# Kernel tuning notes

Hardware: AMD Instinct MI355X
Metric: run time of the kernel (lower is better)

Reference implementation:

```python
import jax, jax.numpy as jnp
import numpy as np

NEG_SLOPE = 0.2
HEADS = 8

def _gat_conv(x, src, dst, n_nodes, W, att_src, att_dst, bias):
    # x: [N, Fin], W: [Fin, H*C], att_*: [H, C], bias: [C]
    H, C = att_src.shape
    xl = (x @ W).reshape(n_nodes, H, C)                      # [N,H,C]
    a_src = (xl * att_src[None]).sum(-1)                      # [N,H]
    a_dst = (xl * att_dst[None]).sum(-1)                      # [N,H]
    e = jax.nn.leaky_relu(a_src[src] + a_dst[dst], NEG_SLOPE) # [E,H]
    m = jax.ops.segment_max(e, dst, num_segments=n_nodes)     # [N,H]
    ee = jnp.exp(e - m[dst])
    s = jax.ops.segment_sum(ee, dst, num_segments=n_nodes)    # [N,H]
    alpha = ee / s[dst]                                       # [E,H]
    msg = alpha[:, :, None] * xl[src]                         # [E,H,C]
    out = jax.ops.segment_sum(msg, dst, num_segments=n_nodes) # [N,H,C]
    return out.mean(axis=1) + bias                            # [N,C] (concat=False)

def setup_inputs() -> dict:
    key = jax.random.key(0)
    ks = jax.random.split(key, 12)
    N, E, EL = 50000, 800000, 200000
    V, D, HID, OUT = 5000, 128, 32, 32
    inp = {}
    inp['x'] = jax.random.randint(ks[0], (N,), 0, V)
    inp['edge_index'] = jax.random.randint(ks[1], (2, E), 0, N)
    inp['edge_label_index'] = jax.random.randint(ks[2], (2, EL), 0, N)
    inp['emb'] = jax.random.normal(ks[3], (V, D), jnp.float32) * D ** -0.5
    inp['W1'] = jax.random.normal(ks[4], (D, HEADS * HID), jnp.float32) * D ** -0.5
    inp['att_src1'] = jax.random.normal(ks[5], (HEADS, HID), jnp.float32) * HID ** -0.5
    inp['att_dst1'] = jax.random.normal(ks[6], (HEADS, HID), jnp.float32) * HID ** -0.5
    inp['b1'] = jnp.zeros((HID,), jnp.float32)
    inp['W2'] = jax.random.normal(ks[7], (HID, HEADS * OUT), jnp.float32) * HID ** -0.5
    inp['att_src2'] = jax.random.normal(ks[8], (HEADS, OUT), jnp.float32) * OUT ** -0.5
    inp['att_dst2'] = jax.random.normal(ks[9], (HEADS, OUT), jnp.float32) * OUT ** -0.5
    inp['b2'] = jnp.zeros((OUT,), jnp.float32)
    return inp

def reference(x, edge_index, edge_label_index, emb, W1, att_src1, att_dst1, b1, W2, att_src2, att_dst2, b2):
    N = x.shape[0]
    # PyG GATConv adds self-loops by default
    loop = jnp.arange(N)
    src = jnp.concatenate([edge_index[0], loop])
    dst = jnp.concatenate([edge_index[1], loop])
    h = emb[x]                                                   # [N, D] embedding lookup (squeeze(1) equivalent)
    h = jax.nn.relu(_gat_conv(h, src, dst, N, W1, att_src1, att_dst1, b1))
    # dropout p=0.5 is identity at inference (training=False)
    z = _gat_conv(h, src, dst, N, W2, att_src2, att_dst2, b2)    # [N, OUT]
    # decode: dot product over label edges
    return (z[edge_label_index[0]] * z[edge_label_index[1]]).sum(axis=-1)
```

## Files before the change

### kernel.cpp

```cpp
#include <hip/hip_runtime.h>
#include <hip/hip_fp16.h>
#include <math.h>
#include <limits.h>

#define HH 8
#define CC 32
#define NEG 0.2f

struct __align__(8) half4 { __half2 a, b; };
typedef float f32x4 __attribute__((ext_vector_type(4)));

__device__ __forceinline__ int ldnt(const int* p){ return __builtin_nontemporal_load(p); }
__device__ __forceinline__ float ldntf(const float* p){ return __builtin_nontemporal_load(p); }
__device__ __forceinline__ f32x4 ldnt4(const float* p){ return __builtin_nontemporal_load((const f32x4*)p); }
__device__ __forceinline__ void stnt4(float* p, f32x4 v){ __builtin_nontemporal_store(v, (f32x4*)p); }
__device__ __forceinline__ int f2ord(float f){ int i=__float_as_int(f); return i>=0? i : i^0x7fffffff; }
__device__ __forceinline__ float ord2f(int i){ return __int_as_float(i>=0? i : i^0x7fffffff); }

__device__ __forceinline__ void edge_sd_nt(const int* __restrict__ ei, int e, int E, int& s, int& d){
  if(e < E){ s = ldnt(ei+e); d = ldnt(ei+E+e); } else { s = e-E; d = s; }
}

__global__ void k_init2(int* __restrict__ cnt, int* __restrict__ gmax, int N){
  int i = blockIdx.x*blockDim.x + threadIdx.x;
  if(i < N) cnt[i] = 0;
  if(i < 16) gmax[i] = INT_MIN;
}

__global__ void k_count(const int* __restrict__ ei, int E, int ET, int* __restrict__ cnt){
  int e = blockIdx.x*blockDim.x + threadIdx.x;
  if(e >= ET) return;
  int d = (e < E) ? ldnt(ei+E+e) : e-E;
  atomicAdd(&cnt[d], 1);
}

__global__ __launch_bounds__(256) void k_scan_block(const int* __restrict__ cnt,
                                                    int* __restrict__ off,
                                                    int* __restrict__ bsum, int N){
  int i = blockIdx.x*256 + threadIdx.x;
  int v = (i < N) ? cnt[i] : 0;
  int lane = threadIdx.x & 63;
  int incl = v;
  #pragma unroll
  for(int o=1;o<64;o<<=1){ int u = __shfl_up(incl,o); if(lane>=o) incl += u; }
  __shared__ int wsum[4];
  if(lane==63) wsum[threadIdx.x>>6] = incl;
  __syncthreads();
  int w = threadIdx.x>>6, wadd = 0;
  #pragma unroll
  for(int k=0;k<4;k++) if(k<w) wadd += wsum[k];
  if(i < N) off[i] = wadd + incl - v;
  if(threadIdx.x==255) bsum[blockIdx.x] = wadd + incl;
}

__global__ __launch_bounds__(256) void k_scan_bsum(int* __restrict__ bsum, int nb,
                                                   int* __restrict__ offN){
  int t = threadIdx.x;
  int v = (t < nb) ? bsum[t] : 0;
  int lane = t & 63;
  int incl = v;
  #pragma unroll
  for(int o=1;o<64;o<<=1){ int u = __shfl_up(incl,o); if(lane>=o) incl += u; }
  __shared__ int wsum[4];
  if(lane==63) wsum[t>>6] = incl;
  __syncthreads();
  int w = t>>6, wadd = 0;
  #pragma unroll
  for(int k=0;k<4;k++) if(k<w) wadd += wsum[k];
  if(t < nb) bsum[t] = wadd + incl - v;
  if(t == 255) *offN = wadd + incl;
}

__global__ void k_scan_add(int* __restrict__ off, const int* __restrict__ bsum,
                           int* __restrict__ cur, int N){
  int i = blockIdx.x*256 + threadIdx.x;
  if(i < N){ int v = off[i] + bsum[blockIdx.x]; off[i] = v; cur[i] = v; }
}

__global__ void k_scatter(const int* __restrict__ ei, int E, int ET,
                          const int* __restrict__ x,
                          int* __restrict__ cur, int* __restrict__ csr_src,
                          int* __restrict__ csr_xv){
  int e = blockIdx.x*blockDim.x + threadIdx.x;
  if(e >= ET) return;
  int s,d; edge_sd_nt(ei,e,E,s,d);
  int pos = atomicAdd(&cur[d], 1);
  csr_src[pos] = s;
  csr_xv[pos]  = x[s];
}

__global__ __launch_bounds__(256) void k_ws(const float* __restrict__ W2,
                                            const float* __restrict__ att_s2,
                                            const float* __restrict__ att_d2,
                                            float* __restrict__ ws_s, float* __restrict__ ws_d){
  int k = threadIdx.x >> 3, h = threadIdx.x & 7;
  float ss = 0.f, dd = 0.f;
  for(int c=0;c<CC;c++){
    float w = W2[k*256 + h*CC + c];
    ss = fmaf(w, att_s2[h*CC+c], ss);
    dd = fmaf(w, att_d2[h*CC+c], dd);
  }
  ws_s[k*HH+h] = ss;
  ws_d[k*HH+h] = dd;
}

__global__ __launch_bounds__(256) void k_gmax(const float* __restrict__ a, int n8,
                                              int* __restrict__ gmax){
  int tid = blockIdx.x*256 + threadIdx.x;
  int lane = threadIdx.x & 63;
  float m = -INFINITY;
  for(int i = tid; i < n8; i += gridDim.x*256) m = fmaxf(m, a[i]);
  #pragma unroll
  for(int msk=8; msk<64; msk<<=1) m = fmaxf(m, __shfl_xor(m, msk));
  if(lane < 8) atomicMax(&gmax[lane], f2ord(m));
}

__global__ void k_adst1(const int* __restrict__ x, const float* __restrict__ a_dst_v,
                        float* __restrict__ adst1, int N8){
  int i = blockIdx.x*256 + threadIdx.x;
  if(i >= N8) return;
  adst1[i] = a_dst_v[x[i>>3]*HH + (i&7)];
}

__global__ __launch_bounds__(256,4) void k_gemm1(
    const float* __restrict__ X, const float* __restrict__ W,
    const float* __restrict__ att_s, const float* __restrict__ att_d,
    __half* __restrict__ xl, float* __restrict__ a_src, float* __restrict__ a_dst,
    int* __restrict__ gmax1, int V){
  const int ROWS = 8, FIN = 128;
  __shared__ __align__(16) float xs[ROWS][FIN];
  __shared__ int smax[8];
  int row0 = blockIdx.x*ROWS;
  int tid = threadIdx.x;
  if(tid < 8) smax[tid] = INT_MIN;
  for(int p = tid; p < ROWS*FIN; p += 256){
    int r = p/FIN, kk = p - r*FIN;
    int row = row0 + r;
    xs[r][kk] = (row < V) ? ldntf(X + (size_t)row*FIN + kk) : 0.f;
  }
  __syncthreads();
  float acc[ROWS];
  #pragma unroll
  for(int r=0;r<ROWS;r++) acc[r]=0.f;
  for(int k=0;k<FIN;k++){
    float w = W[(size_t)k*256 + tid];
    #pragma unroll
    for(int r=0;r<ROWS;r++) acc[r] = fmaf(xs[r][k], w, acc[r]);
  }
  float as = att_s[tid], ad = att_d[tid];
  #pragma unroll
  for(int r=0;r<ROWS;r++){
    int n = row0+r;
    float v = acc[r];
    float ps = v*as, pd = v*ad;
    #pragma unroll
    for(int msk=16; msk>=1; msk>>=1){
      ps += __shfl_xor(ps, msk);
      pd += __shfl_xor(pd, msk);
    }
    if(n < V){
      xl[(size_t)n*256 + tid] = __float2half(v);
      if((tid&31)==0){
        int hh = tid>>5;
        a_src[n*HH+hh] = ps;
        a_dst[n*HH+hh] = pd;
        atomicMax(&smax[hh], f2ord(ps));
      }
    }
  }
  __syncthreads();
  if(tid < 8) atomicMax(&gmax1[tid], smax[tid]);
}

__global__ __launch_bounds__(256) void k_fused1(
    const int* __restrict__ off, const int* __restrict__ csr_xv,
    const float* __restrict__ a_src_v, const float* __restrict__ adst1,
    const int* __restrict__ gmax1,
    const __half* __restrict__ xl_v, const float* __restrict__ bias,
    const float* __restrict__ ws_s, const float* __restrict__ ws_d,
    __half* __restrict__ h2h, float* __restrict__ a_src2, float* __restrict__ a_dst2, int N){
  int wid = (int)((blockIdx.x*(size_t)blockDim.x + threadIdx.x) >> 6);
  int lane = threadIdx.x & 63;
  if(wid >= N) return;
  const int start = off[wid], end = off[wid+1];
  const int t = lane >> 3, h = lane & 7;
  const float ad = adst1[wid*HH + h];
  float mb = ord2f(gmax1[h]) + ad;
  mb = mb > 0.f ? mb : NEG*mb;

  const int h2 = lane >> 3, q = lane & 7, c0 = q*4;
  const __half* xp = xl_v + h2*CC + c0;

  int sv = ldnt(csr_xv + min(start + t, end-1));
  float sraw = a_src_v[sv*HH + h] + ad;
  bool valid = (start + t) < end;

  float eesum = 0.f;
  float4 acc = make_float4(0.f,0.f,0.f,0.f);
  for(int j0 = start; j0 < end; j0 += 8){
    int svn = 0; float srawn = 0.f; bool validn = false;
    if(j0 + 8 < end){
      int jjn = j0 + 8 + t;
      svn = ldnt(csr_xv + min(jjn, end-1));
      srawn = a_src_v[svn*HH + h] + ad;
      validn = jjn < end;
    }
    float v = sraw > 0.f ? sraw : NEG*sraw;
    float ee = valid ? __expf(v - mb) : 0.f;
    eesum += ee;
    float av[8];
    #pragma unroll
    for(int u=0;u<8;u++) av[u] = __shfl(ee, u*8 + h2);
    int s0 = __builtin_amdgcn_readlane(sv, 0);
    int s1 = __builtin_amdgcn_readlane(sv, 8);
    int s2 = __builtin_amdgcn_readlane(sv, 16);
    int s3 = __builtin_amdgcn_readlane(sv, 24);
    int s4 = __builtin_amdgcn_readlane(sv, 32);
    int s5 = __builtin_amdgcn_readlane(sv, 40);
    int s6 = __builtin_amdgcn_readlane(sv, 48);
    int s7 = __builtin_amdgcn_readlane(sv, 56);
    uint2 rv[8];
    rv[0] = *reinterpret_cast<const uint2*>(xp + (size_t)s0*256);
    rv[1] = *reinterpret_cast<const uint2*>(xp + (size_t)s1*256);
    rv[2] = *reinterpret_cast<const uint2*>(xp + (size_t)s2*256);
    rv[3] = *reinterpret_cast<const uint2*>(xp + (size_t)s3*256);
    rv[4] = *reinterpret_cast<const uint2*>(xp + (size_t)s4*256);
    rv[5] = *reinterpret_cast<const uint2*>(xp + (size_t)s5*256);
    rv[6] = *reinterpret_cast<const uint2*>(xp + (size_t)s6*256);
    rv[7] = *reinterpret_cast<const uint2*>(xp + (size_t)s7*256);
    #pragma unroll
    for(int u=0;u<8;u++){
      __half2 ha = *reinterpret_cast<__half2*>(&rv[u].x);
      __half2 hb = *reinterpret_cast<__half2*>(&rv[u].y);
      float2 f01 = __half22float2(ha), f23 = __half22float2(hb);
      acc.x = fmaf(av[u], f01.x, acc.x);
      acc.y = fmaf(av[u], f01.y, acc.y);
      acc.z = fmaf(av[u], f23.x, acc.z);
      acc.w = fmaf(av[u], f23.y, acc.w);
    }
    sv = svn; sraw = srawn; valid = validn;
  }
  #pragma unroll
  for(int msk=8; msk<64; msk<<=1) eesum += __shfl_xor(eesum, msk);
  float is2 = 0.125f / __shfl(eesum, h2);
  acc.x *= is2; acc.y *= is2; acc.z *= is2; acc.w *= is2;
  #pragma unroll
  for(int msk=8; msk<64; msk<<=1){
    acc.x += __shfl_xor(acc.x, msk);
    acc.y += __shfl_xor(acc.y, msk);
    acc.z += __shfl_xor(acc.z, msk);
    acc.w += __shfl_xor(acc.w, msk);
  }
  const float4 b = *reinterpret_cast<const float4*>(bias + c0);
  float4 o = make_float4(fmaxf(acc.x+b.x,0.f), fmaxf(acc.y+b.y,0.f),
                         fmaxf(acc.z+b.z,0.f), fmaxf(acc.w+b.w,0.f));
  if(lane < 8){
    half4 hv;
    hv.a = __floats2half2_rn(o.x, o.y);
    hv.b = __floats2half2_rn(o.z, o.w);
    *reinterpret_cast<half4*>(h2h + (size_t)wid*CC + c0) = hv;
  }
  float ps, pd;
  ps  = o.x * ws_s[(4*q+0)*HH + h2];
  ps = fmaf(o.y, ws_s[(4*q+1)*HH + h2], ps);
  ps = fmaf(o.z, ws_s[(4*q+2)*HH + h2], ps);
  ps = fmaf(o.w, ws_s[(4*q+3)*HH + h2], ps);
  pd  = o.x * ws_d[(4*q+0)*HH + h2];
  pd = fmaf(o.y, ws_d[(4*q+1)*HH + h2], pd);
  pd = fmaf(o.z, ws_d[(4*q+2)*HH + h2], pd);
  pd = fmaf(o.w, ws_d[(4*q+3)*HH + h2], pd);
  #pragma unroll
  for(int msk=1; msk<8; msk<<=1){
    ps += __shfl_xor(ps, msk);
    pd += __shfl_xor(pd, msk);
  }
  if(q == 0){
    a_src2[wid*HH + h2] = ps;
    a_dst2[wid*HH + h2] = pd;
  }
}

__global__ __launch_bounds__(256) void k_agg2(
    const int* __restrict__ off, const int* __restrict__ csr_src,
    const float* __restrict__ a_src2, const float* __restrict__ a_dst2,
    const int* __restrict__ gmax2,
    const __half* __restrict__ h2h, float* __restrict__ agg, int N){
  int wid = (int)((blockIdx.x*(size_t)blockDim.x + threadIdx.x) >> 6);
  int lane = threadIdx.x & 63;
  if(wid >= N) return;
  const int start = off[wid], end = off[wid+1];
  const int t = lane >> 3, h = lane & 7;
  const float ad = a_dst2[wid*HH + h];
  float mb = ord2f(gmax2[h]) + ad;
  mb = mb > 0.f ? mb : NEG*mb;

  const int h2 = lane >> 3, k0 = (lane & 7)*4;
  const __half* hp = h2h + k0;

  int sv = ldnt(csr_src + min(start + t, end-1));
  float sraw = a_src2[sv*HH + h] + ad;
  bool valid = (start + t) < end;

  float eesum = 0.f;
  float4 acc = make_float4(0.f,0.f,0.f,0.f);
  for(int j0 = start; j0 < end; j0 += 8){
    int svn = 0; float srawn = 0.f; bool validn = false;
    if(j0 + 8 < end){
      int jjn = j0 + 8 + t;
      svn = ldnt(csr_src + min(jjn, end-1));
      srawn = a_src2[svn*HH + h] + ad;
      validn = jjn < end;
    }
    float v = sraw > 0.f ? sraw : NEG*sraw;
    float ee = valid ? __expf(v - mb) : 0.f;
    eesum += ee;
    float av[8];
    #pragma unroll
    for(int u=0;u<8;u++) av[u] = __shfl(ee, u*8 + h2);
    int s0 = __builtin_amdgcn_readlane(sv, 0);
    int s1 = __builtin_amdgcn_readlane(sv, 8);
    int s2 = __builtin_amdgcn_readlane(sv, 16);
    int s3 = __builtin_amdgcn_readlane(sv, 24);
    int s4 = __builtin_amdgcn_readlane(sv, 32);
    int s5 = __builtin_amdgcn_readlane(sv, 40);
    int s6 = __builtin_amdgcn_readlane(sv, 48);
    int s7 = __builtin_amdgcn_readlane(sv, 56);
    uint2 rv[8];
    rv[0] = *reinterpret_cast<const uint2*>(hp + (size_t)s0*CC);
    rv[1] = *reinterpret_cast<const uint2*>(hp + (size_t)s1*CC);
    rv[2] = *reinterpret_cast<const uint2*>(hp + (size_t)s2*CC);
    rv[3] = *reinterpret_cast<const uint2*>(hp + (size_t)s3*CC);
    rv[4] = *reinterpret_cast<const uint2*>(hp + (size_t)s4*CC);
    rv[5] = *reinterpret_cast<const uint2*>(hp + (size_t)s5*CC);
    rv[6] = *reinterpret_cast<const uint2*>(hp + (size_t)s6*CC);
    rv[7] = *reinterpret_cast<const uint2*>(hp + (size_t)s7*CC);
    #pragma unroll
    for(int u=0;u<8;u++){
      __half2 ha = *reinterpret_cast<__half2*>(&rv[u].x);
      __half2 hb = *reinterpret_cast<__half2*>(&rv[u].y);
      float2 f01 = __half22float2(ha), f23 = __half22float2(hb);
      acc.x = fmaf(av[u], f01.x, acc.x);
      acc.y = fmaf(av[u], f01.y, acc.y);
      acc.z = fmaf(av[u], f23.x, acc.z);
      acc.w = fmaf(av[u], f23.y, acc.w);
    }
    sv = svn; sraw = srawn; valid = validn;
  }
  #pragma unroll
  for(int msk=8; msk<64; msk<<=1) eesum += __shfl_xor(eesum, msk);
  float is2 = 0.125f / __shfl(eesum, h2);
  f32x4 o; o.x = acc.x*is2; o.y = acc.y*is2; o.z = acc.z*is2; o.w = acc.w*is2;
  stnt4(agg + (size_t)wid*256 + lane*4, o);
}

__global__ __launch_bounds__(256) void k_trans2(
    const float* __restrict__ agg, const float* __restrict__ W2,
    const float* __restrict__ b2, float* __restrict__ z, int N){
  __shared__ __align__(16) float aggl[4][256];
  int w = threadIdx.x >> 6, lane = threadIdx.x & 63;
  int wid = (int)(blockIdx.x*4 + w);
  bool active = wid < N;
  f32x4 av = {0.f,0.f,0.f,0.f};
  if(active) av = ldnt4(agg + (size_t)wid*256 + lane*4);
  *reinterpret_cast<f32x4*>(&aggl[w][lane*4]) = av;
  __syncthreads();

  const int ch = lane & 31, part = lane >> 5;
  float p0=0.f, p1=0.f, p2=0.f, p3=0.f;
  #pragma unroll
  for(int hh = 0; hh < 4; ++hh){
    int hq = part*4 + hh;
    const float* wcol = W2 + hq*CC + ch;
    const float* a = &aggl[w][hq*CC];
    #pragma unroll
    for(int k=0;k<CC;k+=4){
      p0 = fmaf(a[k+0], wcol[(size_t)(k+0)*256], p0);
      p1 = fmaf(a[k+1], wcol[(size_t)(k+1)*256], p1);
      p2 = fmaf(a[k+2], wcol[(size_t)(k+2)*256], p2);
      p3 = fmaf(a[k+3], wcol[(size_t)(k+3)*256], p3);
    }
  }
  float p = (p0+p1)+(p2+p3);
  p += __shfl_xor(p, 32);
  if(active && part==0) z[(size_t)wid*CC + ch] = p + b2[ch];
}

__global__ void k_decode(const int* __restrict__ eli, int EL,
                         const float* __restrict__ z, float* __restrict__ out){
  int e = blockIdx.x*blockDim.x + threadIdx.x;
  if(e >= EL) return;
  const float4* za = reinterpret_cast<const float4*>(z + (size_t)ldnt(eli+e)*CC);
  const float4* zb = reinterpret_cast<const float4*>(z + (size_t)ldnt(eli+EL+e)*CC);
  float s = 0.f;
  #pragma unroll
  for(int j=0;j<8;j++){
    float4 u = za[j], v = zb[j];
    s += u.x*v.x + u.y*v.y + u.z*v.z + u.w*v.w;
  }
  out[e] = s;
}

extern "C" void kernel_launch(void* const* d_in, const int* in_sizes, int n_in,
                              void* d_out, int out_size, void* d_ws, size_t ws_size,
                              hipStream_t stream){
  const int*   x   = (const int*)d_in[0];
  const int*   ei  = (const int*)d_in[1];
  const int*   eli = (const int*)d_in[2];
  const float* emb = (const float*)d_in[3];
  const float* W1  = (const float*)d_in[4];
  const float* as1 = (const float*)d_in[5];
  const float* ad1 = (const float*)d_in[6];
  const float* b1  = (const float*)d_in[7];
  const float* W2  = (const float*)d_in[8];
  const float* as2 = (const float*)d_in[9];
  const float* ad2 = (const float*)d_in[10];
  const float* b2  = (const float*)d_in[11];

  const int N  = in_sizes[0];
  const int V  = in_sizes[3]/128;
  const int E  = in_sizes[1]/2;
  const int EL = in_sizes[2]/2;
  const int ET = E + N;

  __half* xl_v = (__half*)d_ws;
  __half* h2h  = xl_v + (size_t)V*256;
  float* a_src_v = (float*)(h2h + (size_t)N*CC);
  float* a_dst_v = a_src_v + (size_t)V*HH;
  float* adst1   = a_dst_v + (size_t)V*HH;
  float* a_src2  = adst1 + (size_t)N*HH;
  float* a_dst2  = a_src2 + (size_t)N*HH;
  float* z       = a_dst2 + (size_t)N*HH;
  float* agg     = z + (size_t)N*CC;
  float* ws_s    = agg + (size_t)N*256;
  float* ws_d    = ws_s + 256;
  int*   gmax1   = (int*)(ws_d + 256);
  int*   gmax2   = gmax1 + 8;
  int*   cnt   = gmax2 + 8;
  int*   off   = cnt + N;
  int*   cur   = off + N + 1;
  int*   bsum  = cur + N;
  int*   csr   = bsum + ((N+255)/256);
  int*   csr_xv= csr + ET;

  dim3 blk(256);
  auto cdiv = [](long long a, long long b){ return (unsigned)((a+b-1)/b); };
  const int nb = (int)cdiv(N,256);

  k_init2<<<cdiv(N,256), blk, 0, stream>>>(cnt, gmax1, N);
  k_count<<<cdiv(ET,256), blk, 0, stream>>>(ei, E, ET, cnt);
  k_scan_block<<<nb, blk, 0, stream>>>(cnt, off, bsum, N);
  k_scan_bsum<<<1, blk, 0, stream>>>(bsum, nb, off + N);
  k_scan_add<<<nb, blk, 0, stream>>>(off, bsum, cur, N);
  k_scatter<<<cdiv(ET,256), blk, 0, stream>>>(ei, E, ET, x, cur, csr, csr_xv);

  k_ws<<<1, blk, 0, stream>>>(W2, as2, ad2, ws_s, ws_d);

  k_gemm1<<<cdiv(V,8), blk, 0, stream>>>(emb, W1, as1, ad1, xl_v, a_src_v, a_dst_v, gmax1, V);
  k_adst1<<<cdiv((long long)N*HH,256), blk, 0, stream>>>(x, a_dst_v, adst1, N*HH);
  k_fused1<<<cdiv((long long)N*64,256), blk, 0, stream>>>(off, csr_xv, a_src_v, adst1,
                                                          gmax1, xl_v, b1, ws_s, ws_d,
                                                          h2h, a_src2, a_dst2, N);

  k_gmax<<<64, blk, 0, stream>>>(a_src2, N*HH, gmax2);
  k_agg2<<<cdiv((long long)N*64,256), blk, 0, stream>>>(off, csr, a_src2, a_dst2,
                                                        gmax2, h2h, agg, N);
  k_trans2<<<cdiv(N,4), blk, 0, stream>>>(agg, W2, b2, z, N);

  k_decode<<<cdiv(EL,256), blk, 0, stream>>>(eli, EL, z, (float*)d_out);
}
```

Measured before the change: 337.2 us.

## Fuse layer-2 aggregation with W2 transform through per-wave LDS staging

Merges k_agg2 and k_trans2 into one kernel, k_fused2. Each wave now writes its normalized 256-wide aggregate into its own shared-memory row and immediately runs the W2 projection to produce z. This removes the N×256 fp32 intermediate buffer, which cost a global write plus a read back, and drops one kernel launch. The block-wide __syncthreads goes away because each wave touches only its own LDS row, which relies on intra-wave ordering of LDS accesses.

```diff
diff --git a/kernel.cpp b/kernel.cpp
--- a/kernel.cpp
+++ b/kernel.cpp
@@ -12,8 +12,6 @@
 
 __device__ __forceinline__ int ldnt(const int* p){ return __builtin_nontemporal_load(p); }
 __device__ __forceinline__ float ldntf(const float* p){ return __builtin_nontemporal_load(p); }
-__device__ __forceinline__ f32x4 ldnt4(const float* p){ return __builtin_nontemporal_load((const f32x4*)p); }
-__device__ __forceinline__ void stnt4(float* p, f32x4 v){ __builtin_nontemporal_store(v, (f32x4*)p); }
 __device__ __forceinline__ int f2ord(float f){ int i=__float_as_int(f); return i>=0? i : i^0x7fffffff; }
 __device__ __forceinline__ float ord2f(int i){ return __int_as_float(i>=0? i : i^0x7fffffff); }
 
@@ -280,11 +278,14 @@
   }
 }
 
-__global__ __launch_bounds__(256) void k_agg2(
+__global__ __launch_bounds__(256) void k_fused2(
     const int* __restrict__ off, const int* __restrict__ csr_src,
     const float* __restrict__ a_src2, const float* __restrict__ a_dst2,
     const int* __restrict__ gmax2,
-    const __half* __restrict__ h2h, float* __restrict__ agg, int N){
+    const __half* __restrict__ h2h, const float* __restrict__ W2,
+    const float* __restrict__ b2, float* __restrict__ z, int N){
+  __shared__ __align__(16) float aggl[4][256];
+  int w = threadIdx.x >> 6;
   int wid = (int)((blockIdx.x*(size_t)blockDim.x + threadIdx.x) >> 6);
   int lane = threadIdx.x & 63;
   if(wid >= N) return;
@@ -349,40 +350,27 @@
   #pragma unroll
   for(int msk=8; msk<64; msk<<=1) eesum += __shfl_xor(eesum, msk);
   float is2 = 0.125f / __shfl(eesum, h2);
-  f32x4 o; o.x = acc.x*is2; o.y = acc.y*is2; o.z = acc.z*is2; o.w = acc.w*is2;
-  stnt4(agg + (size_t)wid*256 + lane*4, o);
-}
-
-__global__ __launch_bounds__(256) void k_trans2(
-    const float* __restrict__ agg, const float* __restrict__ W2,
-    const float* __restrict__ b2, float* __restrict__ z, int N){
-  __shared__ __align__(16) float aggl[4][256];
-  int w = threadIdx.x >> 6, lane = threadIdx.x & 63;
-  int wid = (int)(blockIdx.x*4 + w);
-  bool active = wid < N;
-  f32x4 av = {0.f,0.f,0.f,0.f};
-  if(active) av = ldnt4(agg + (size_t)wid*256 + lane*4);
-  *reinterpret_cast<f32x4*>(&aggl[w][lane*4]) = av;
-  __syncthreads();
-
+  f32x4 oo; oo.x = acc.x*is2; oo.y = acc.y*is2; oo.z = acc.z*is2; oo.w = acc.w*is2;
+  *reinterpret_cast<f32x4*>(&aggl[w][h2*CC + k0]) = oo;
   const int ch = lane & 31, part = lane >> 5;
+  const f32x4* arow4 = reinterpret_cast<const f32x4*>(&aggl[w][0]);
   float p0=0.f, p1=0.f, p2=0.f, p3=0.f;
   #pragma unroll
   for(int hh = 0; hh < 4; ++hh){
     int hq = part*4 + hh;
     const float* wcol = W2 + hq*CC + ch;
-    const float* a = &aggl[w][hq*CC];
-    #pragma unroll
-    for(int k=0;k<CC;k+=4){
-      p0 = fmaf(a[k+0], wcol[(size_t)(k+0)*256], p0);
-      p1 = fmaf(a[k+1], wcol[(size_t)(k+1)*256], p1);
-      p2 = fmaf(a[k+2], wcol[(size_t)(k+2)*256], p2);
-      p3 = fmaf(a[k+3], wcol[(size_t)(k+3)*256], p3);
+    #pragma unroll
+    for(int k4=0; k4<8; ++k4){
+      f32x4 a4 = arow4[hq*8 + k4];
+      p0 = fmaf(a4.x, wcol[(size_t)(4*k4+0)*256], p0);
+      p1 = fmaf(a4.y, wcol[(size_t)(4*k4+1)*256], p1);
+      p2 = fmaf(a4.z, wcol[(size_t)(4*k4+2)*256], p2);
+      p3 = fmaf(a4.w, wcol[(size_t)(4*k4+3)*256], p3);
     }
   }
   float p = (p0+p1)+(p2+p3);
   p += __shfl_xor(p, 32);
-  if(active && part==0) z[(size_t)wid*CC + ch] = p + b2[ch];
+  if(part==0) z[(size_t)wid*CC + ch] = p + b2[ch];
 }
 
 __global__ void k_decode(const int* __restrict__ eli, int EL,
@@ -430,8 +418,7 @@
   float* a_src2  = adst1 + (size_t)N*HH;
   float* a_dst2  = a_src2 + (size_t)N*HH;
   float* z       = a_dst2 + (size_t)N*HH;
-  float* agg     = z + (size_t)N*CC;
-  float* ws_s    = agg + (size_t)N*256;
+  float* ws_s    = z + (size_t)N*CC;
   float* ws_d    = ws_s + 256;
   int*   gmax1   = (int*)(ws_d + 256);
   int*   gmax2   = gmax1 + 8;
@@ -462,9 +449,8 @@
                                                           h2h, a_src2, a_dst2, N);
 
   k_gmax<<<64, blk, 0, stream>>>(a_src2, N*HH, gmax2);
-  k_agg2<<<cdiv((long long)N*64,256), blk, 0, stream>>>(off, csr, a_src2, a_dst2,
-                                                        gmax2, h2h, agg, N);
-  k_trans2<<<cdiv(N,4), blk, 0, stream>>>(agg, W2, b2, z, N);
+  k_fused2<<<cdiv((long long)N*64,256), blk, 0, stream>>>(off, csr, a_src2, a_dst2,
+                                                          gmax2, h2h, W2, b2, z, N);
 
   k_decode<<<cdiv(EL,256), blk, 0, stream>>>(eli, EL, z, (float*)d_out);
 }
```

Result: faster. 300.1 us (-11.0%).
